# Kernel tuning notes

Measured on AMD Instinct MI355X. Metric: run time of the kernel, lower is better.

## Reference

```python
import jax, jax.numpy as jnp
import numpy as np

ERR = 1e-12


def setup_inputs() -> dict:
    key = jax.random.key(0)
    k1, k2, k3 = jax.random.split(key, 3)
    B, H, L, D = 2, 16, 2048, 64
    k = jax.random.normal(k1, (B, H, L, D), dtype=jnp.float32)
    src = jax.random.uniform(k2, (B, H, L), dtype=jnp.float32)
    dest = jax.random.uniform(k3, (B, H, L), dtype=jnp.float32)
    return {"k": k, "src": src, "dest": dest}


def reference(k, src, dest):
    # k: [B,H,L,D], src/dest: [B,H,L]
    L = k.shape[-2]
    s = jnp.sqrt(src + ERR)   # sqrt-scaled source weights
    d = jnp.sqrt(dest + ERR)  # sqrt-scaled destination weights
    # affinity_1[b,h,i,j] = s_i * d_j * (k_i . k_j), fused as (k*s) @ (k*d)^T
    a1 = jnp.einsum("bhid,bhjd->bhij", k * s[..., :, None], k * d[..., :, None])
    # relu then (x+err)^(2/3)  (kernel: exp2(log2(relu(a)+err) * 2/3))
    a3 = jnp.exp2(jnp.log2(jax.nn.relu(a1) + ERR) * (2.0 / 3.0))
    # forward cumulative sum over j, output causally masked to j >= i
    cs = jnp.cumsum(a3, axis=-1)
    idx = jnp.arange(L)
    mask = idx[:, None] <= idx[None, :]  # keep j >= i
    return jnp.where(mask, cs, 0.0)
```

## Files before the change

kernel.cpp:

```cpp
#include <hip/hip_runtime.h>

#define BH   32
#define LSEQ 2048
#define DDIM 64
#define ERRC 1e-12f

typedef __attribute__((ext_vector_type(8))) short  bf16x8;
typedef __attribute__((ext_vector_type(4))) float  floatx4;
typedef __attribute__((ext_vector_type(4))) unsigned short ushort4v;

__device__ __forceinline__ unsigned short f2bf(float f) {
    unsigned u = __float_as_uint(f);
    u = u + 0x7FFFu + ((u >> 16) & 1u);
    return (unsigned short)(u >> 16);
}

__device__ __forceinline__ bf16x8 pack8s(const float* __restrict__ p, float w) {
    const floatx4* pv = (const floatx4*)p;
    floatx4 x = pv[0], y = pv[1];
    bf16x8 r;
    r[0] = (short)f2bf(x[0] * w); r[1] = (short)f2bf(x[1] * w);
    r[2] = (short)f2bf(x[2] * w); r[3] = (short)f2bf(x[3] * w);
    r[4] = (short)f2bf(y[0] * w); r[5] = (short)f2bf(y[1] * w);
    r[6] = (short)f2bf(y[2] * w); r[7] = (short)f2bf(y[3] * w);
    return r;
}

__global__ __launch_bounds__(256) void prep_scaled(const float* __restrict__ k,
                                                   const float* __restrict__ src,
                                                   const float* __restrict__ dest,
                                                   unsigned short* __restrict__ ks,
                                                   unsigned short* __restrict__ kd) {
    int idx4 = blockIdx.x * 256 + threadIdx.x;
    int row  = idx4 >> 4;
    float s = sqrtf(src[row] + ERRC);
    float d = sqrtf(dest[row] + ERRC);
    floatx4 v = ((const floatx4*)k)[idx4];
    ushort4v os, od;
#pragma unroll
    for (int r = 0; r < 4; ++r) { os[r] = f2bf(v[r] * s); od[r] = f2bf(v[r] * d); }
    ((ushort4v*)ks)[idx4] = os;
    ((ushort4v*)kd)[idx4] = od;
}

template<bool RAW>
__device__ __forceinline__ void load_row(const void* __restrict__ kp, long base, int row,
                                         int q, const float* __restrict__ w, int bhL,
                                         bf16x8& lo, bf16x8& hi) {
    if (RAW) {
        const float* p = (const float*)kp + base + (long)row * DDIM + q * 8;
        float s = sqrtf(w[bhL + row] + ERRC);
        lo = pack8s(p, s);
        hi = pack8s(p + 32, s);
    } else {
        const unsigned short* p = (const unsigned short*)kp + base + (long)row * DDIM + q * 8;
        lo = *(const bf16x8*)p;
        hi = *(const bf16x8*)(p + 32);
    }
}

__device__ __forceinline__ void scan_store(float t[4], int j0, int i0, int q, int l16,
                                           float& carry, float* __restrict__ op) {
    if (j0 + 16 <= i0) {
        float g = (t[0] + t[1]) + (t[2] + t[3]);
        g += __shfl_xor(g, 16, 64);
        g += __shfl_xor(g, 32, 64);
        carry += g;
        floatx4 z = {0.f, 0.f, 0.f, 0.f};
        *(floatx4*)op = z;
    } else {
        t[1] += t[0]; t[2] += t[1]; t[3] += t[2];
        float g = t[3];
        float u1 = __shfl_up(g, 16, 64);
        float h = g + ((q >= 1) ? u1 : 0.f);
        float u2 = __shfl_up(h, 32, 64);
        h += ((q >= 2) ? u2 : 0.f);
        float bse = (h - g) + carry;
        carry += __shfl(h, 48 + l16, 64);
        floatx4 o;
        if (j0 == i0) {
#pragma unroll
            for (int r = 0; r < 4; ++r)
                o[r] = ((q * 4 + r) >= l16) ? (t[r] + bse) : 0.f;
        } else {
#pragma unroll
            for (int r = 0; r < 4; ++r)
                o[r] = t[r] + bse;
        }
        *(floatx4*)op = o;
    }
}

template<bool RAW>
__global__ __launch_bounds__(256) void mha_fused2(const void* __restrict__ ka,
                                                  const void* __restrict__ kb,
                                                  const float* __restrict__ src,
                                                  const float* __restrict__ dest,
                                                  float* __restrict__ out) {
    const int tid  = threadIdx.x;
    const int wave = tid >> 6;
    const int lane = tid & 63;
    const int q    = lane >> 4;
    const int l16  = lane & 15;
    const int bh = blockIdx.x & 31;
    const int ib = blockIdx.x >> 5;
    const int i0 = (ib * 4 + wave) * 16;
    const int bhL = bh * LSEQ;
    const long base = (long)bh * LSEQ * DDIM;

    bf16x8 blo, bhi;
    load_row<RAW>(kb, base, i0 + l16, q, src, bhL, blo, bhi);

    float carry = 0.f;
    const float c23 = 2.0f / 3.0f;

    bf16x8 aAlo, aAhi, aBlo, aBhi;
    load_row<RAW>(ka, base, l16,      q, dest, bhL, aAlo, aAhi);
    load_row<RAW>(ka, base, 16 + l16, q, dest, bhL, aBlo, aBhi);

    float* orow = out + (long)(bhL + i0 + l16) * LSEQ + q * 4;

    for (int jp = 0; jp < 64; ++jp) {
        const int j0A = jp << 5;
        const int j0B = j0A + 16;

        bf16x8 nAlo, nAhi, nBlo, nBhi;
        const int jn = (jp < 63) ? (jp + 1) << 5 : j0A;
        load_row<RAW>(ka, base, jn + l16,      q, dest, bhL, nAlo, nAhi);
        load_row<RAW>(ka, base, jn + 16 + l16, q, dest, bhL, nBlo, nBhi);

        floatx4 accA = {0.f, 0.f, 0.f, 0.f};
        floatx4 accB = {0.f, 0.f, 0.f, 0.f};
        accA = __builtin_amdgcn_mfma_f32_16x16x32_bf16(aAlo, blo, accA, 0, 0, 0);
        accB = __builtin_amdgcn_mfma_f32_16x16x32_bf16(aBlo, blo, accB, 0, 0, 0);
        accA = __builtin_amdgcn_mfma_f32_16x16x32_bf16(aAhi, bhi, accA, 0, 0, 0);
        accB = __builtin_amdgcn_mfma_f32_16x16x32_bf16(aBhi, bhi, accB, 0, 0, 0);

        float tA[4], tB[4];
#pragma unroll
        for (int r = 0; r < 4; ++r) {
            float vA = fmaxf(accA[r], 0.f) + ERRC;
            tA[r] = exp2f(c23 * __log2f(vA));
            float vB = fmaxf(accB[r], 0.f) + ERRC;
            tB[r] = exp2f(c23 * __log2f(vB));
        }

        scan_store(tA, j0A, i0, q, l16, carry, orow);
        scan_store(tB, j0B, i0, q, l16, carry, orow + 16);

        orow += 32;
        aAlo = nAlo; aAhi = nAhi; aBlo = nBlo; aBhi = nBhi;
    }
}

extern "C" void kernel_launch(void* const* d_in, const int* in_sizes, int n_in,
                              void* d_out, int out_size, void* d_ws, size_t ws_size,
                              hipStream_t stream) {
    const float* k    = (const float*)d_in[0];
    const float* src  = (const float*)d_in[1];
    const float* dest = (const float*)d_in[2];
    float* out = (float*)d_out;

    const size_t half = (size_t)BH * LSEQ * DDIM * sizeof(unsigned short);
    if (ws_size >= 2 * half) {
        unsigned short* ks = (unsigned short*)d_ws;
        unsigned short* kd = (unsigned short*)((char*)d_ws + half);
        prep_scaled<<<dim3(4096), dim3(256), 0, stream>>>(k, src, dest, ks, kd);
        mha_fused2<false><<<dim3(1024), dim3(256), 0, stream>>>(kd, ks, src, dest, out);
    } else {
        mha_fused2<true><<<dim3(1024), dim3(256), 0, stream>>>(k, k, src, dest, out);
    }
}
```

Measured before the change: 638.8 us.

## Switch to 32x32x16 MFMA tiles with per-wave 32-row blocks and nontemporal stores

```diff
diff --git a/kernel.cpp b/kernel.cpp
--- a/kernel.cpp
+++ b/kernel.cpp
@@ -5,9 +5,10 @@
 #define DDIM 64
 #define ERRC 1e-12f
 
-typedef __attribute__((ext_vector_type(8))) short  bf16x8;
-typedef __attribute__((ext_vector_type(4))) float  floatx4;
-typedef __attribute__((ext_vector_type(4))) unsigned short ushort4v;
+typedef __attribute__((ext_vector_type(8)))  short bf16x8;
+typedef __attribute__((ext_vector_type(4)))  float floatx4;
+typedef __attribute__((ext_vector_type(16))) float floatx16;
+typedef __attribute__((ext_vector_type(4)))  unsigned short ushort4v;
 
 __device__ __forceinline__ unsigned short f2bf(float f) {
     unsigned u = __float_as_uint(f);
@@ -44,55 +45,23 @@
 }
 
 template<bool RAW>
-__device__ __forceinline__ void load_row(const void* __restrict__ kp, long base, int row,
-                                         int q, const float* __restrict__ w, int bhL,
-                                         bf16x8& lo, bf16x8& hi) {
+__device__ __forceinline__ void load_frags(const void* __restrict__ kp, long base, int row,
+                                           int h, const float* __restrict__ w, int bhL,
+                                           bf16x8& f0, bf16x8& f1, bf16x8& f2, bf16x8& f3) {
     if (RAW) {
-        const float* p = (const float*)kp + base + (long)row * DDIM + q * 8;
+        const float* p = (const float*)kp + base + (long)row * DDIM + h * 8;
         float s = sqrtf(w[bhL + row] + ERRC);
-        lo = pack8s(p, s);
-        hi = pack8s(p + 32, s);
+        f0 = pack8s(p, s);      f1 = pack8s(p + 16, s);
+        f2 = pack8s(p + 32, s); f3 = pack8s(p + 48, s);
     } else {
-        const unsigned short* p = (const unsigned short*)kp + base + (long)row * DDIM + q * 8;
-        lo = *(const bf16x8*)p;
-        hi = *(const bf16x8*)(p + 32);
-    }
-}
-
-__device__ __forceinline__ void scan_store(float t[4], int j0, int i0, int q, int l16,
-                                           float& carry, float* __restrict__ op) {
-    if (j0 + 16 <= i0) {
-        float g = (t[0] + t[1]) + (t[2] + t[3]);
-        g += __shfl_xor(g, 16, 64);
-        g += __shfl_xor(g, 32, 64);
-        carry += g;
-        floatx4 z = {0.f, 0.f, 0.f, 0.f};
-        *(floatx4*)op = z;
-    } else {
-        t[1] += t[0]; t[2] += t[1]; t[3] += t[2];
-        float g = t[3];
-        float u1 = __shfl_up(g, 16, 64);
-        float h = g + ((q >= 1) ? u1 : 0.f);
-        float u2 = __shfl_up(h, 32, 64);
-        h += ((q >= 2) ? u2 : 0.f);
-        float bse = (h - g) + carry;
-        carry += __shfl(h, 48 + l16, 64);
-        floatx4 o;
-        if (j0 == i0) {
-#pragma unroll
-            for (int r = 0; r < 4; ++r)
-                o[r] = ((q * 4 + r) >= l16) ? (t[r] + bse) : 0.f;
-        } else {
-#pragma unroll
-            for (int r = 0; r < 4; ++r)
-                o[r] = t[r] + bse;
-        }
-        *(floatx4*)op = o;
+        const unsigned short* p = (const unsigned short*)kp + base + (long)row * DDIM + h * 8;
+        f0 = *(const bf16x8*)p;        f1 = *(const bf16x8*)(p + 16);
+        f2 = *(const bf16x8*)(p + 32); f3 = *(const bf16x8*)(p + 48);
     }
 }
 
 template<bool RAW>
-__global__ __launch_bounds__(256) void mha_fused2(const void* __restrict__ ka,
+__global__ __launch_bounds__(256) void mha_fused3(const void* __restrict__ ka,
                                                   const void* __restrict__ kb,
                                                   const float* __restrict__ src,
                                                   const float* __restrict__ dest,
@@ -100,56 +69,102 @@
     const int tid  = threadIdx.x;
     const int wave = tid >> 6;
     const int lane = tid & 63;
-    const int q    = lane >> 4;
-    const int l16  = lane & 15;
+    const int c    = lane & 31;
+    const int h    = lane >> 5;
     const int bh = blockIdx.x & 31;
     const int ib = blockIdx.x >> 5;
-    const int i0 = (ib * 4 + wave) * 16;
+    const int i0 = (ib * 4 + wave) * 32;
     const int bhL = bh * LSEQ;
     const long base = (long)bh * LSEQ * DDIM;
 
-    bf16x8 blo, bhi;
-    load_row<RAW>(kb, base, i0 + l16, q, src, bhL, blo, bhi);
+    bf16x8 b0, b1, b2, b3;
+    load_frags<RAW>(kb, base, i0 + c, h, src, bhL, b0, b1, b2, b3);
 
     float carry = 0.f;
     const float c23 = 2.0f / 3.0f;
 
-    bf16x8 aAlo, aAhi, aBlo, aBhi;
-    load_row<RAW>(ka, base, l16,      q, dest, bhL, aAlo, aAhi);
-    load_row<RAW>(ka, base, 16 + l16, q, dest, bhL, aBlo, aBhi);
+    bf16x8 a0, a1, a2, a3;
+    load_frags<RAW>(ka, base, c, h, dest, bhL, a0, a1, a2, a3);
 
-    float* orow = out + (long)(bhL + i0 + l16) * LSEQ + q * 4;
+    float* orow = out + (long)(bhL + i0 + c) * LSEQ + 4 * h;
 
-    for (int jp = 0; jp < 64; ++jp) {
-        const int j0A = jp << 5;
-        const int j0B = j0A + 16;
+    for (int jt = 0; jt < 64; ++jt) {
+        const int j0 = jt << 5;
 
-        bf16x8 nAlo, nAhi, nBlo, nBhi;
-        const int jn = (jp < 63) ? (jp + 1) << 5 : j0A;
-        load_row<RAW>(ka, base, jn + l16,      q, dest, bhL, nAlo, nAhi);
-        load_row<RAW>(ka, base, jn + 16 + l16, q, dest, bhL, nBlo, nBhi);
+        bf16x8 n0, n1, n2, n3;
+        const int jn = (jt < 63) ? (jt + 1) << 5 : 0;
+        load_frags<RAW>(ka, base, jn + c, h, dest, bhL, n0, n1, n2, n3);
 
-        floatx4 accA = {0.f, 0.f, 0.f, 0.f};
-        floatx4 accB = {0.f, 0.f, 0.f, 0.f};
-        accA = __builtin_amdgcn_mfma_f32_16x16x32_bf16(aAlo, blo, accA, 0, 0, 0);
-        accB = __builtin_amdgcn_mfma_f32_16x16x32_bf16(aBlo, blo, accB, 0, 0, 0);
-        accA = __builtin_amdgcn_mfma_f32_16x16x32_bf16(aAhi, bhi, accA, 0, 0, 0);
-        accB = __builtin_amdgcn_mfma_f32_16x16x32_bf16(aBhi, bhi, accB, 0, 0, 0);
+        floatx16 acc;
+#pragma unroll
+        for (int e = 0; e < 16; ++e) acc[e] = 0.f;
+        acc = __builtin_amdgcn_mfma_f32_32x32x16_bf16(a0, b0, acc, 0, 0, 0);
+        acc = __builtin_amdgcn_mfma_f32_32x32x16_bf16(a1, b1, acc, 0, 0, 0);
+        acc = __builtin_amdgcn_mfma_f32_32x32x16_bf16(a2, b2, acc, 0, 0, 0);
+        acc = __builtin_amdgcn_mfma_f32_32x32x16_bf16(a3, b3, acc, 0, 0, 0);
 
-        float tA[4], tB[4];
+        float u[16];
 #pragma unroll
-        for (int r = 0; r < 4; ++r) {
-            float vA = fmaxf(accA[r], 0.f) + ERRC;
-            tA[r] = exp2f(c23 * __log2f(vA));
-            float vB = fmaxf(accB[r], 0.f) + ERRC;
-            tB[r] = exp2f(c23 * __log2f(vB));
+        for (int e = 0; e < 16; ++e) {
+            float v = fmaxf(acc[e], 0.f) + ERRC;
+            u[e] = exp2f(c23 * __log2f(v));
         }
 
-        scan_store(tA, j0A, i0, q, l16, carry, orow);
-        scan_store(tB, j0B, i0, q, l16, carry, orow + 16);
+        if (j0 + 32 <= i0) {
+            float s = (((u[0] + u[1]) + (u[2] + u[3])) + ((u[4] + u[5]) + (u[6] + u[7])))
+                    + (((u[8] + u[9]) + (u[10] + u[11])) + ((u[12] + u[13]) + (u[14] + u[15])));
+            carry += s + __shfl_xor(s, 32, 64);
+            const floatx4 z = {0.f, 0.f, 0.f, 0.f};
+#pragma unroll
+            for (int g = 0; g < 4; ++g)
+                __builtin_nontemporal_store(z, (floatx4*)(orow + 8 * g));
+        } else {
+#pragma unroll
+            for (int g = 0; g < 4; ++g) {
+                u[4 * g + 1] += u[4 * g + 0];
+                u[4 * g + 2] += u[4 * g + 1];
+                u[4 * g + 3] += u[4 * g + 2];
+            }
+            const float S0 = u[3], S1 = u[7], S2 = u[11], S3 = u[15];
+            const float P0 = __shfl_xor(S0, 32, 64);
+            const float P1 = __shfl_xor(S1, 32, 64);
+            const float P2 = __shfl_xor(S2, 32, 64);
+            const float P3 = __shfl_xor(S3, 32, 64);
+            const float q0 = S0 + P0, q1 = S1 + P1, q2 = S2 + P2, q3 = S3 + P3;
+            const float e0 = carry;
+            const float e1 = e0 + q0;
+            const float e2 = e1 + q1;
+            const float e3 = e2 + q2;
+            carry = e3 + q3;
+            const float hx = (h != 0) ? 1.f : 0.f;
+            const float E0 = e0 + hx * P0, E1 = e1 + hx * P1,
+                        E2 = e2 + hx * P2, E3 = e3 + hx * P3;
+
+            if (j0 == i0) {
+#pragma unroll
+                for (int g = 0; g < 4; ++g) {
+                    const float Eg = (g == 0) ? E0 : (g == 1) ? E1 : (g == 2) ? E2 : E3;
+                    floatx4 o;
+#pragma unroll
+                    for (int r = 0; r < 4; ++r)
+                        o[r] = ((8 * g + 4 * h + r) >= c) ? (u[4 * g + r] + Eg) : 0.f;
+                    __builtin_nontemporal_store(o, (floatx4*)(orow + 8 * g));
+                }
+            } else {
+#pragma unroll
+                for (int g = 0; g < 4; ++g) {
+                    const float Eg = (g == 0) ? E0 : (g == 1) ? E1 : (g == 2) ? E2 : E3;
+                    floatx4 o;
+#pragma unroll
+                    for (int r = 0; r < 4; ++r)
+                        o[r] = u[4 * g + r] + Eg;
+                    __builtin_nontemporal_store(o, (floatx4*)(orow + 8 * g));
+                }
+            }
+        }
 
         orow += 32;
-        aAlo = nAlo; aAhi = nAhi; aBlo = nBlo; aBhi = nBhi;
+        a0 = n0; a1 = n1; a2 = n2; a3 = n3;
     }
 }
 
@@ -166,8 +181,8 @@
         unsigned short* ks = (unsigned short*)d_ws;
         unsigned short* kd = (unsigned short*)((char*)d_ws + half);
         prep_scaled<<<dim3(4096), dim3(256), 0, stream>>>(k, src, dest, ks, kd);
-        mha_fused2<false><<<dim3(1024), dim3(256), 0, stream>>>(kd, ks, src, dest, out);
+        mha_fused3<false><<<dim3(512), dim3(256), 0, stream>>>(kd, ks, src, dest, out);
     } else {
-        mha_fused2<true><<<dim3(1024), dim3(256), 0, stream>>>(k, k, src, dest, out);
+        mha_fused3<true><<<dim3(512), dim3(256), 0, stream>>>(k, k, src, dest, out);
     }
 }
```

New measurement: 1.136 ms. 1.78x slower.
